# Kernel optimization log

Measured on AMD Instinct MI355X. Metric: run time of the kernel, lower is better.

Reference implementation:

```python
import jax, jax.numpy as jnp
import numpy as np

V = 6890   # SMPL vertices
K = 24     # joints
NB = 10    # shape betas
NP = 207   # pose blendshape basis = 23*9
PARENTS = np.array([-1, 0, 0, 0, 1, 2, 3, 4, 5, 6, 7, 8, 9, 9, 9, 12, 13, 14, 16, 17, 18, 19, 20, 21])


def setup_inputs() -> dict:
    key = jax.random.key(0)
    ks = jax.random.split(key, 8)
    B = 1024
    body_pose = jax.random.normal(ks[0], (B, 69), dtype=jnp.float32) * 0.2
    betas = jax.random.normal(ks[1], (B, NB), dtype=jnp.float32)
    global_orient = jax.random.normal(ks[2], (B, 3), dtype=jnp.float32) * 0.2
    v_template = jax.random.normal(ks[3], (V, 3), dtype=jnp.float32) * 0.1
    shapedirs = jax.random.normal(ks[4], (V, 3, NB), dtype=jnp.float32) * 0.01
    posedirs = jax.random.normal(ks[5], (NP, V * 3), dtype=jnp.float32) * 0.01
    J_regressor = jax.nn.softmax(jax.random.normal(ks[6], (K, V), dtype=jnp.float32), axis=-1)
    lbs_weights = jax.nn.softmax(jax.random.normal(ks[7], (V, K), dtype=jnp.float32) * 4.0, axis=-1)
    parents = jnp.asarray(PARENTS, dtype=jnp.int32)
    return dict(body_pose=body_pose, betas=betas, global_orient=global_orient,
                v_template=v_template, shapedirs=shapedirs, posedirs=posedirs,
                J_regressor=J_regressor, lbs_weights=lbs_weights, parents=parents)


def _rodrigues(aa):
    # aa: [..., 3] axis-angle -> [..., 3, 3] rotation matrices
    angle = jnp.linalg.norm(aa + 1e-8, axis=-1, keepdims=True)  # [...,1]
    axis = aa / angle
    sin = jnp.sin(angle)[..., None]
    cos = jnp.cos(angle)[..., None]
    rx, ry, rz = axis[..., 0], axis[..., 1], axis[..., 2]
    z = jnp.zeros_like(rx)
    Km = jnp.stack([z, -rz, ry, rz, z, -rx, -ry, rx, z], axis=-1).reshape(aa.shape[:-1] + (3, 3))
    ident = jnp.eye(3, dtype=aa.dtype)
    return ident + sin * Km + (1.0 - cos) * (Km @ Km)


def reference(body_pose, betas, global_orient, v_template, shapedirs, posedirs,
              J_regressor, lbs_weights, parents):
    full_pose = jnp.concatenate([global_orient, body_pose], axis=1)  # [B,72]
    B = betas.shape[0]
    dtype = betas.dtype

    # shape blend shapes
    v_shaped = v_template + jnp.einsum('bl,vkl->bvk', betas, shapedirs)  # [B,V,3]
    # rest joints
    joints_t = jnp.einsum('jv,bvk->bjk', J_regressor, v_shaped)          # [B,K,3]

    # pose -> rotation matrices (pose2rot=True path)
    rot_mats = _rodrigues(full_pose.reshape(B, K, 3))                    # [B,K,3,3]

    # pose blend shapes
    ident = jnp.eye(3, dtype=dtype)
    pose_feature = (rot_mats[:, 1:] - ident).reshape(B, NP)              # [B,207]
    v_posed = v_shaped + (pose_feature @ posedirs).reshape(B, V, 3)

    # kinematic chain (batch_rigid_transform)
    rel_joints = joints_t.at[:, 1:].add(-joints_t[:, PARENTS[1:]])       # [B,K,3]
    tm = jnp.concatenate([rot_mats, rel_joints[..., None]], axis=-1)     # [B,K,3,4]
    bottom = jnp.broadcast_to(jnp.array([0., 0., 0., 1.], dtype=dtype), (B, K, 1, 4))
    tm = jnp.concatenate([tm, bottom], axis=-2)                          # [B,K,4,4]
    chain = [tm[:, 0]]
    for i in range(1, K):  # fixed small kinematic tree
        chain.append(chain[PARENTS[i]] @ tm[:, i])
    transforms = jnp.stack(chain, axis=1)                                # [B,K,4,4]
    joints = transforms[..., :3, 3]                                      # posed joints

    # relative transforms: subtract rotated rest-joint position
    A = transforms.at[..., :3, 3].add(
        -jnp.einsum('bkij,bkj->bki', transforms[..., :3, :3], joints_t))  # [B,K,4,4]

    # linear blend skinning
    T = jnp.einsum('vk,bkij->bvij', lbs_weights, A)                      # [B,V,4,4]
    vertices = jnp.einsum('bvij,bvj->bvi', T[..., :3, :3], v_posed) + T[..., :3, 3]
    return vertices, joints_t, joints, rot_mats
```

## Files before the change

kernel.cpp:

```cpp
#include <hip/hip_runtime.h>
#include <hip/hip_bf16.h>

#define VNUM 6890
#define KJ 24
#define NBETA 10
#define NPOSE 207
#define KPAD 224
#define BATCH 1024
#define N3 20670
#define N3PAD 20672
#define VPAD 6912

#define OUT_V  0
#define OUT_JT 21166080
#define OUT_J  21239808
#define OUT_RM 21313536

#define WS_JVJS 0
#define WS_ABF  792
#define WS_WBF  246552
#define WS_PFB  384792
#define WS_PDT  499480

typedef unsigned short ushort;
typedef __attribute__((ext_vector_type(8))) short short8v;
typedef __attribute__((ext_vector_type(4))) float floatx4;

__device__ __forceinline__ ushort f2bfu(float x) {
  __hip_bfloat16 h = __float2bfloat16(x);
  union { __hip_bfloat16 h; ushort u; } cv; cv.h = h; return cv.u;
}

__global__ __launch_bounds__(256) void jreg_kernel(
    const float* __restrict__ Jr, const float* __restrict__ vt,
    const float* __restrict__ sd, float* __restrict__ JvJs) {
  const int j = blockIdx.x;
  const int chunk = blockIdx.y;
  const int t = threadIdx.x;
  const int lane = t & 63, wid = t >> 6;
  const int vbeg = chunk * 1723;
  const int vend = (vbeg + 1723 < VNUM) ? vbeg + 1723 : VNUM;
  __shared__ float red[4][33];
  float acc[33];
#pragma unroll
  for (int q = 0; q < 33; q++) acc[q] = 0.0f;
  for (int v = vbeg + t; v < vend; v += 256) {
    float r = Jr[j * VNUM + v];
    const float* vtp = vt + v * 3;
    const float* sdp = sd + v * 30;
    acc[0] += r * vtp[0];
    acc[1] += r * vtp[1];
    acc[2] += r * vtp[2];
#pragma unroll
    for (int q = 0; q < 30; q++) acc[3 + q] += r * sdp[q];
  }
#pragma unroll
  for (int q = 0; q < 33; q++) {
    float x = acc[q];
    for (int off = 32; off > 0; off >>= 1) x += __shfl_down(x, off, 64);
    if (lane == 0) red[wid][q] = x;
  }
  __syncthreads();
  if (t < 33)
    atomicAdd(&JvJs[j * 33 + t], red[0][t] + red[1][t] + red[2][t] + red[3][t]);
}

__global__ __launch_bounds__(64) void batch_prep(
    const float* __restrict__ body_pose, const float* __restrict__ betas,
    const float* __restrict__ global_orient, const float* __restrict__ JvJs,
    float* __restrict__ out_jt, float* __restrict__ out_j, float* __restrict__ out_rm,
    ushort* __restrict__ pfb, ushort* __restrict__ Abf) {
  const int b = blockIdx.x;
  const int t = threadIdx.x;
  __shared__ float R[24][9];
  __shared__ float jt[24][3];
  __shared__ float chR[24][9];
  __shared__ float cht[24][3];

  if (t < 24) {
    float ax, ay, az;
    if (t == 0) {
      ax = global_orient[b * 3 + 0];
      ay = global_orient[b * 3 + 1];
      az = global_orient[b * 3 + 2];
    } else {
      const float* p = body_pose + (size_t)b * 69 + (t - 1) * 3;
      ax = p[0]; ay = p[1]; az = p[2];
    }
    float px = ax + 1e-8f, py = ay + 1e-8f, pz = az + 1e-8f;
    float angle = sqrtf(px * px + py * py + pz * pz);
    float inv = 1.0f / angle;
    float rx = ax * inv, ry = ay * inv, rz = az * inv;
    float s = sinf(angle), c = cosf(angle);
    float cc = 1.0f - c;
    float m[9];
    m[0] = 1.0f - cc * (ry * ry + rz * rz);
    m[1] = -s * rz + cc * rx * ry;
    m[2] =  s * ry + cc * rx * rz;
    m[3] =  s * rz + cc * rx * ry;
    m[4] = 1.0f - cc * (rx * rx + rz * rz);
    m[5] = -s * rx + cc * ry * rz;
    m[6] = -s * ry + cc * rx * rz;
    m[7] =  s * rx + cc * ry * rz;
    m[8] = 1.0f - cc * (rx * rx + ry * ry);
#pragma unroll
    for (int e = 0; e < 9; e++) {
      R[t][e] = m[e];
      out_rm[(size_t)b * 216 + t * 9 + e] = m[e];
    }
  }
  for (int idx = t; idx < 72; idx += 64) {
    int j = idx / 3, c = idx % 3;
    const float* JJ = JvJs + j * 33;
    float s = JJ[c];
    const float* be = betas + (size_t)b * NBETA;
#pragma unroll
    for (int l = 0; l < NBETA; l++) s += be[l] * JJ[3 + c * 10 + l];
    jt[j][c] = s;
    out_jt[(size_t)b * 72 + idx] = s;
  }
  __syncthreads();
  for (int mI = t; mI < KPAD; mI += 64) {
    float val = 0.0f;
    if (mI < NPOSE) {
      int k = 1 + mI / 9, e = mI % 9;
      val = R[k][e] - ((e == 0 || e == 4 || e == 8) ? 1.0f : 0.0f);
    } else if (mI < NPOSE + NBETA) {
      val = betas[(size_t)b * NBETA + (mI - NPOSE)];
    }
    pfb[(size_t)b * KPAD + mI] = f2bfu(val);
  }
  if (t == 0) {
    const int par[24] = {-1, 0, 0, 0, 1, 2, 3, 4, 5, 6, 7, 8, 9, 9, 9, 12, 13, 14, 16, 17, 18, 19, 20, 21};
#pragma unroll
    for (int e = 0; e < 9; e++) chR[0][e] = R[0][e];
    cht[0][0] = jt[0][0]; cht[0][1] = jt[0][1]; cht[0][2] = jt[0][2];
    for (int k = 1; k < 24; k++) {
      int p = par[k];
      float rel0 = jt[k][0] - jt[p][0];
      float rel1 = jt[k][1] - jt[p][1];
      float rel2 = jt[k][2] - jt[p][2];
#pragma unroll
      for (int i = 0; i < 3; i++) {
        float a0 = chR[p][i * 3 + 0], a1 = chR[p][i * 3 + 1], a2 = chR[p][i * 3 + 2];
        chR[k][i * 3 + 0] = a0 * R[k][0] + a1 * R[k][3] + a2 * R[k][6];
        chR[k][i * 3 + 1] = a0 * R[k][1] + a1 * R[k][4] + a2 * R[k][7];
        chR[k][i * 3 + 2] = a0 * R[k][2] + a1 * R[k][5] + a2 * R[k][8];
        cht[k][i] = a0 * rel0 + a1 * rel1 + a2 * rel2 + cht[p][i];
      }
    }
  }
  __syncthreads();
  if (t < 24) {
    int k = t;
#pragma unroll
    for (int i = 0; i < 3; i++) out_j[(size_t)b * 72 + k * 3 + i] = cht[k][i];
  }
  for (int e = t; e < 480; e += 64) {
    int n = e / 40, k = e - (e / 40) * 40;
    float val = 0.0f;
    if (k < 24) {
      int i = n >> 2, jj = n & 3;
      if (jj < 3) {
        val = chR[k][i * 3 + jj];
      } else {
        val = cht[k][i] - (chR[k][i * 3 + 0] * jt[k][0] +
                           chR[k][i * 3 + 1] * jt[k][1] +
                           chR[k][i * 3 + 2] * jt[k][2]);
      }
    }
    Abf[(size_t)b * 480 + e] = f2bfu(val);
  }
}

__global__ __launch_bounds__(256) void transpose_pd(
    const float* __restrict__ pd, ushort* __restrict__ pdT,
    const float* __restrict__ sd,
    const float* __restrict__ w, ushort* __restrict__ wbf) {
  {
    int lb = blockIdx.y * 323 + blockIdx.x;
    if (lb < 1080) {
      int i = lb * 256 + threadIdx.x;
      int v = i / 40, k = i - v * 40;
      float x = (v < VNUM && k < 24) ? w[v * 24 + k] : 0.0f;
      wbf[i] = f2bfu(x);
    }
  }
  __shared__ float tile[32][65];
  const int t = threadIdx.x;
  const int n0 = blockIdx.x * 64;
  const int k0 = blockIdx.y * 32;
  const int c = t & 63;
  for (int r = t >> 6; r < 32; r += 4) {
    int k = k0 + r, n = n0 + c;
    float x = 0.0f;
    if (n < N3) {
      if (k < NPOSE) x = pd[(size_t)k * N3 + n];
      else if (k < NPOSE + NBETA) x = sd[(size_t)n * 10 + (k - NPOSE)];
    }
    tile[r][c] = x;
  }
  __syncthreads();
  const int n = t >> 2;
  const int j0 = (t & 3) * 8;
  unsigned int outw[4];
#pragma unroll
  for (int jj = 0; jj < 4; jj++) {
    unsigned int lo = f2bfu(tile[j0 + jj * 2][n]);
    unsigned int hi = f2bfu(tile[j0 + jj * 2 + 1][n]);
    outw[jj] = lo | (hi << 16);
  }
  *(uint4*)&pdT[(size_t)(n0 + n) * KPAD + k0 + j0] =
      make_uint4(outw[0], outw[1], outw[2], outw[3]);
}

__global__ __launch_bounds__(256, 4) void fused_mfma(
    const ushort* __restrict__ pfb, const ushort* __restrict__ pdT,
    const float* __restrict__ vt, const ushort* __restrict__ wbf,
    const ushort* __restrict__ Abf, float* __restrict__ out_v) {
  __shared__ __align__(16) ushort Bs[48 * KPAD];
  __shared__ float vpS[64 * 50];
  __shared__ float vtS[48];
  const int tid = threadIdx.x;
  const int lane = tid & 63, wv = tid >> 6;
  const int l15 = lane & 15, quad = lane >> 4;
  const int bm = blockIdx.x * 64;
  const int v0 = blockIdx.y * 16;

  const short8v wf = *(const short8v*)(wbf + (size_t)(v0 + l15) * 40 + quad * 8);

  short8v av[7];
  const ushort* arow = pfb + (size_t)(bm + wv * 16 + l15) * KPAD;
#pragma unroll
  for (int kb = 0; kb < 7; kb++)
    av[kb] = *(const short8v*)(arow + kb * 32 + quad * 8);

  {
    const uint4* src = (const uint4*)pdT;
    uint4* dB = (uint4*)Bs;
    for (int e = tid; e < 48 * 28; e += 256) {
      int row = e / 28, q = e - row * 28;
      int n = v0 * 3 + row;
      if (n >= N3PAD) n = 0;
      dB[row * 28 + q] = src[(size_t)n * 28 + q];
    }
    if (tid < 48) {
      int gn = v0 * 3 + tid;
      vtS[tid] = (gn < N3) ? vt[gn] : 0.0f;
    }
  }
  __syncthreads();

  floatx4 acc[3];
  const floatx4 zero = {0.0f, 0.0f, 0.0f, 0.0f};
#pragma unroll
  for (int ns = 0; ns < 3; ns++) acc[ns] = zero;
#pragma unroll
  for (int kb = 0; kb < 7; kb++) {
#pragma unroll
    for (int ns = 0; ns < 3; ns++) {
      short8v bv = *(const short8v*)&Bs[(ns * 16 + l15) * KPAD + kb * 32 + quad * 8];
      acc[ns] = __builtin_amdgcn_mfma_f32_16x16x32_bf16(av[kb], bv, acc[ns], 0, 0, 0);
    }
  }
#pragma unroll
  for (int ns = 0; ns < 3; ns++) {
    int col = ns * 16 + l15;
    float vtv = vtS[col];
#pragma unroll
    for (int r = 0; r < 4; r++)
      vpS[(wv * 16 + quad * 4 + r) * 50 + col] = acc[ns][r] + vtv;
  }
  __builtin_amdgcn_sched_barrier(0);
  __builtin_amdgcn_s_waitcnt(0xc07f);
  __builtin_amdgcn_sched_barrier(0);

  const int gv = v0 + l15;
  const bool active = (quad < 3) && (gv < VNUM);
  const size_t vbase = (size_t)gv * 3;
  const ushort* abase = Abf + (size_t)(bm + wv * 16) * 480 + l15 * 40 + quad * 8;

  short8v apre[4];
#pragma unroll
  for (int i = 0; i < 4; i++) apre[i] = *(const short8v*)(abase + i * 480);

#pragma unroll
  for (int i = 0; i < 16; i++) {
    const int b = wv * 16 + i;
    const size_t gb = (size_t)(bm + b);
    short8v afrag = apre[i & 3];
    if (i < 12) apre[i & 3] = *(const short8v*)(abase + (i + 4) * 480);
    floatx4 t = zero;
    t = __builtin_amdgcn_mfma_f32_16x16x32_bf16(afrag, wf, t, 0, 0, 0);
    float px = vpS[b * 50 + 3 * l15 + 0];
    float py = vpS[b * 50 + 3 * l15 + 1];
    float pz = vpS[b * 50 + 3 * l15 + 2];
    if (active) {
      out_v[gb * N3 + vbase + quad] = t[0] * px + t[1] * py + t[2] * pz + t[3];
    }
  }
}

extern "C" void kernel_launch(void* const* d_in, const int* in_sizes, int n_in,
                              void* d_out, int out_size, void* d_ws, size_t ws_size,
                              hipStream_t stream) {
  const float* body_pose     = (const float*)d_in[0];
  const float* betas         = (const float*)d_in[1];
  const float* global_orient = (const float*)d_in[2];
  const float* v_template    = (const float*)d_in[3];
  const float* shapedirs     = (const float*)d_in[4];
  const float* posedirs      = (const float*)d_in[5];
  const float* J_regressor   = (const float*)d_in[6];
  const float* lbs_weights   = (const float*)d_in[7];

  float* out = (float*)d_out;
  float* out_v  = out + OUT_V;
  float* out_jt = out + OUT_JT;
  float* out_j  = out + OUT_J;
  float* out_rm = out + OUT_RM;

  float* ws = (float*)d_ws;
  float* JvJs = ws + WS_JVJS;
  ushort* Abf = (ushort*)(ws + WS_ABF);
  ushort* wbf = (ushort*)(ws + WS_WBF);
  ushort* pfb = (ushort*)(ws + WS_PFB);
  ushort* pdT = (ushort*)(ws + WS_PDT);

  hipMemsetAsync(JvJs, 0, KJ * 33 * sizeof(float), stream);
  jreg_kernel<<<dim3(KJ, 4), 256, 0, stream>>>(J_regressor, v_template, shapedirs, JvJs);
  transpose_pd<<<dim3(323, 7), 256, 0, stream>>>(posedirs, pdT, shapedirs,
                                                 lbs_weights, wbf);
  batch_prep<<<BATCH, 64, 0, stream>>>(body_pose, betas, global_orient, JvJs,
                                       out_jt, out_j, out_rm, pfb, Abf);
  fused_mfma<<<dim3(16, 431), 256, 0, stream>>>(pfb, pdT, v_template, wbf,
                                                Abf, out_v);
}
```

Before: 201.9 us.

## Drop LDS staging of posedirs, shrink blocks, and swizzle block order

The fused kernel no longer stages the posedirs tile in shared memory. Each wave now streams its A and B fragments straight from global memory inside the K loop. Blocks shrink to 128 threads covering 32 batch rows, and a 1D grid uses an XCD-aware swizzle so neighbouring blocks share vertex tiles in cache. This removes the LDS copy and the block barrier and raises occupancy, at the cost of redundant global and L2 reads of the B tiles across waves and blocks.

```diff
diff --git a/kernel.cpp b/kernel.cpp
--- a/kernel.cpp
+++ b/kernel.cpp
@@ -214,89 +214,81 @@
       make_uint4(outw[0], outw[1], outw[2], outw[3]);
 }
 
-__global__ __launch_bounds__(256, 4) void fused_mfma(
+__global__ __launch_bounds__(128, 8) void fused_mfma(
     const ushort* __restrict__ pfb, const ushort* __restrict__ pdT,
     const float* __restrict__ vt, const ushort* __restrict__ wbf,
     const ushort* __restrict__ Abf, float* __restrict__ out_v) {
-  __shared__ __align__(16) ushort Bs[48 * KPAD];
-  __shared__ float vpS[64 * 50];
-  __shared__ float vtS[48];
+  __shared__ float vpS[32 * 50];
   const int tid = threadIdx.x;
   const int lane = tid & 63, wv = tid >> 6;
   const int l15 = lane & 15, quad = lane >> 4;
-  const int bm = blockIdx.x * 64;
-  const int v0 = blockIdx.y * 16;
-
-  const short8v wf = *(const short8v*)(wbf + (size_t)(v0 + l15) * 40 + quad * 8);
-
-  short8v av[7];
-  const ushort* arow = pfb + (size_t)(bm + wv * 16 + l15) * KPAD;
-#pragma unroll
-  for (int kb = 0; kb < 7; kb++)
-    av[kb] = *(const short8v*)(arow + kb * 32 + quad * 8);
-
-  {
-    const uint4* src = (const uint4*)pdT;
-    uint4* dB = (uint4*)Bs;
-    for (int e = tid; e < 48 * 28; e += 256) {
-      int row = e / 28, q = e - row * 28;
-      int n = v0 * 3 + row;
-      if (n >= N3PAD) n = 0;
-      dB[row * 28 + q] = src[(size_t)n * 28 + q];
-    }
-    if (tid < 48) {
-      int gn = v0 * 3 + tid;
-      vtS[tid] = (gn < N3) ? vt[gn] : 0.0f;
-    }
-  }
-  __syncthreads();
-
-  floatx4 acc[3];
-  const floatx4 zero = {0.0f, 0.0f, 0.0f, 0.0f};
-#pragma unroll
-  for (int ns = 0; ns < 3; ns++) acc[ns] = zero;
+
+  const int bid = blockIdx.x;
+  const int L = (bid & 7) * 1724 + (bid >> 3);
+  const int bm = (L & 31) * 32 + wv * 16;
+  const int v0 = (L >> 5) * 16;
+
+  const int gn0 = v0 * 3 + l15;
+  int r0 = gn0;       if (r0 >= N3PAD) r0 = 0;
+  int r1 = gn0 + 16;  if (r1 >= N3PAD) r1 = 0;
+  int r2 = gn0 + 32;  if (r2 >= N3PAD) r2 = 0;
+  const ushort* ap  = pfb + (size_t)(bm + l15) * KPAD + quad * 8;
+  const ushort* bp0 = pdT + (size_t)r0 * KPAD + quad * 8;
+  const ushort* bp1 = pdT + (size_t)r1 * KPAD + quad * 8;
+  const ushort* bp2 = pdT + (size_t)r2 * KPAD + quad * 8;
+
+  floatx4 acc0 = {0.0f, 0.0f, 0.0f, 0.0f};
+  floatx4 acc1 = acc0, acc2 = acc0;
 #pragma unroll
   for (int kb = 0; kb < 7; kb++) {
-#pragma unroll
-    for (int ns = 0; ns < 3; ns++) {
-      short8v bv = *(const short8v*)&Bs[(ns * 16 + l15) * KPAD + kb * 32 + quad * 8];
-      acc[ns] = __builtin_amdgcn_mfma_f32_16x16x32_bf16(av[kb], bv, acc[ns], 0, 0, 0);
-    }
-  }
-#pragma unroll
-  for (int ns = 0; ns < 3; ns++) {
-    int col = ns * 16 + l15;
-    float vtv = vtS[col];
-#pragma unroll
-    for (int r = 0; r < 4; r++)
-      vpS[(wv * 16 + quad * 4 + r) * 50 + col] = acc[ns][r] + vtv;
+    short8v a  = *(const short8v*)(ap  + kb * 32);
+    short8v b0 = *(const short8v*)(bp0 + kb * 32);
+    short8v b1 = *(const short8v*)(bp1 + kb * 32);
+    short8v b2 = *(const short8v*)(bp2 + kb * 32);
+    acc0 = __builtin_amdgcn_mfma_f32_16x16x32_bf16(a, b0, acc0, 0, 0, 0);
+    acc1 = __builtin_amdgcn_mfma_f32_16x16x32_bf16(a, b1, acc1, 0, 0, 0);
+    acc2 = __builtin_amdgcn_mfma_f32_16x16x32_bf16(a, b2, acc2, 0, 0, 0);
+  }
+
+  float vt0 = (gn0      < N3) ? vt[gn0]      : 0.0f;
+  float vt1 = (gn0 + 16 < N3) ? vt[gn0 + 16] : 0.0f;
+  float vt2 = (gn0 + 32 < N3) ? vt[gn0 + 32] : 0.0f;
+
+  float* myvp = &vpS[wv * 16 * 50];
+#pragma unroll
+  for (int r = 0; r < 4; r++) {
+    int row = quad * 4 + r;
+    myvp[row * 50 +      l15] = acc0[r] + vt0;
+    myvp[row * 50 + 16 + l15] = acc1[r] + vt1;
+    myvp[row * 50 + 32 + l15] = acc2[r] + vt2;
   }
   __builtin_amdgcn_sched_barrier(0);
   __builtin_amdgcn_s_waitcnt(0xc07f);
   __builtin_amdgcn_sched_barrier(0);
 
+  const short8v wf = *(const short8v*)(wbf + (size_t)(v0 + l15) * 40 + quad * 8);
   const int gv = v0 + l15;
   const bool active = (quad < 3) && (gv < VNUM);
   const size_t vbase = (size_t)gv * 3;
-  const ushort* abase = Abf + (size_t)(bm + wv * 16) * 480 + l15 * 40 + quad * 8;
+  const ushort* abase = Abf + (size_t)bm * 480 + l15 * 40 + quad * 8;
 
   short8v apre[4];
 #pragma unroll
   for (int i = 0; i < 4; i++) apre[i] = *(const short8v*)(abase + i * 480);
 
+  const floatx4 zero = {0.0f, 0.0f, 0.0f, 0.0f};
 #pragma unroll
   for (int i = 0; i < 16; i++) {
-    const int b = wv * 16 + i;
-    const size_t gb = (size_t)(bm + b);
     short8v afrag = apre[i & 3];
     if (i < 12) apre[i & 3] = *(const short8v*)(abase + (i + 4) * 480);
     floatx4 t = zero;
     t = __builtin_amdgcn_mfma_f32_16x16x32_bf16(afrag, wf, t, 0, 0, 0);
-    float px = vpS[b * 50 + 3 * l15 + 0];
-    float py = vpS[b * 50 + 3 * l15 + 1];
-    float pz = vpS[b * 50 + 3 * l15 + 2];
+    float px = myvp[i * 50 + 3 * l15 + 0];
+    float py = myvp[i * 50 + 3 * l15 + 1];
+    float pz = myvp[i * 50 + 3 * l15 + 2];
     if (active) {
-      out_v[gb * N3 + vbase + quad] = t[0] * px + t[1] * py + t[2] * pz + t[3];
+      out_v[(size_t)(bm + i) * N3 + vbase + quad] =
+          t[0] * px + t[1] * py + t[2] * pz + t[3];
     }
   }
 }
@@ -332,6 +324,5 @@
                                                  lbs_weights, wbf);
   batch_prep<<<BATCH, 64, 0, stream>>>(body_pose, betas, global_orient, JvJs,
                                        out_jt, out_j, out_rm, pfb, Abf);
-  fused_mfma<<<dim3(16, 431), 256, 0, stream>>>(pfb, pdT, v_template, wbf,
-                                                Abf, out_v);
-}
+  fused_mfma<<<13792, 128, 0, stream>>>(pfb, pdT, v_template, wbf, Abf, out_v);
+}
```

After: 226.2 us. +12.0%, slower.
